# Kernel optimization log

Measured on AMD Instinct MI355X. Metric: run time of the kernel, lower is better.

## Reference

```python
import jax, jax.numpy as jnp
import numpy as np

B, N, D = 8, 2048, 512
S = 4096  # max_swaps


def setup_inputs() -> dict:
    key = jax.random.key(0)
    ks = jax.random.split(key, 5)
    h = jax.random.normal(ks[0], (B, N, D), dtype=jnp.float32)
    indices = jax.random.randint(ks[1], (B, S, 4), 0, N, dtype=jnp.int64)
    # MLP params (Linear stores weight as (out,in) in torch; we keep (in,out) and matmul)
    W1 = jax.random.normal(ks[2], (4 * D, D), dtype=jnp.float32) * (1.0 / np.sqrt(4 * D))
    b1 = jnp.zeros((D,), dtype=jnp.float32)
    W2 = jax.random.normal(ks[3], (D, D // 2), dtype=jnp.float32) * (1.0 / np.sqrt(D))
    b2 = jnp.zeros((D // 2,), dtype=jnp.float32)
    W3 = jax.random.normal(ks[4], (D // 2, 1), dtype=jnp.float32) * (1.0 / np.sqrt(D // 2))
    b3 = jnp.zeros((1,), dtype=jnp.float32)
    return {"h": h, "indices": indices, "W1": W1, "b1": b1, "W2": W2, "b2": b2, "W3": W3, "b3": b3}


def reference(h, indices, W1, b1, W2, b2, W3, b3):
    # h: (B, N, D); indices: (B, S, 4) node ids per swap
    swap_emb = jnp.take_along_axis(h[:, None, :, :], indices[..., None].astype(jnp.int32),
                                   axis=2)  # broadcast-gather -> (B, S, 4, D)
    # equivalently: h[batch_idx, indices]; implemented as per-batch gather
    swap_emb = jax.vmap(lambda hb, ib: hb[ib])(h, indices)  # (B, S, 4, D)
    swap_feats = swap_emb.reshape(h.shape[0], indices.shape[1], -1)  # (B, S, 4D)
    x = jax.nn.gelu(swap_feats @ W1 + b1, approximate=False)
    x = jax.nn.gelu(x @ W2 + b2, approximate=False)
    scores = (x @ W3 + b3)[..., 0]  # (B, S)
    rates = jax.nn.softplus(scores)
    return rates
```

## Files before the change

kernel.cpp:

```cpp
#include <hip/hip_runtime.h>
#include <math.h>

#define BATCH 8
#define NNODES 2048
#define DDIM 512
#define SWAPS 4096
#define M_TOTAL (BATCH * SWAPS)
#define KD DDIM
#define K2 DDIM
#define N2 (DDIM / 2)

typedef __attribute__((ext_vector_type(8))) __bf16 bf16x8;
typedef __attribute__((ext_vector_type(4))) float f32x4;
typedef __attribute__((ext_vector_type(8))) unsigned short us8;
typedef unsigned short ushort_t;

__device__ __forceinline__ float gelu_exact(float x) {
    return 0.5f * x * (1.0f + erff(x * 0.70710678118654752440f));
}
__device__ __forceinline__ float softplus_f(float x) {
    return fmaxf(x, 0.0f) + log1pf(expf(-fabsf(x)));
}
__device__ __forceinline__ unsigned short f2bf(float f) {
    unsigned int u = __builtin_bit_cast(unsigned int, f);
    u += 0x7FFFu + ((u >> 16) & 1u);
    return (unsigned short)(u >> 16);
}
__device__ __forceinline__ float bf2f(unsigned short s) {
    return __builtin_bit_cast(float, (unsigned int)s << 16);
}
__device__ __forceinline__ void glds16(const void* g, void* l) {
    __builtin_amdgcn_global_load_lds(
        (const __attribute__((address_space(1))) void*)g,
        (__attribute__((address_space(3))) void*)l, 16, 0, 0);
}

__global__ __launch_bounds__(256) void convert_kernel(
    const float* __restrict__ h, const float* __restrict__ W1,
    const float* __restrict__ W2, ushort_t* __restrict__ h_bf,
    ushort_t* __restrict__ W1pt, ushort_t* __restrict__ W2t)
{
    const int bid = blockIdx.x;
    if (bid < 8192) {
        size_t i = ((size_t)bid * 256 + threadIdx.x) * 4;
        float4 v = *(const float4*)(h + i);
        ushort4 o = { f2bf(v.x), f2bf(v.y), f2bf(v.z), f2bf(v.w) };
        *(ushort4*)(h_bf + i) = o;
    } else if (bid < 8192 + 1024) {
        size_t e = ((size_t)(bid - 8192) * 256 + threadIdx.x) * 4;
        const int k = (int)(e >> 9), n = (int)(e & 511);
        const int sg = k >> 9, d = k & 511;
        const int j = sg * 512 + n;
        float4 v = *(const float4*)(W1 + e);
        W1pt[(size_t)(j + 0) * KD + d] = f2bf(v.x);
        W1pt[(size_t)(j + 1) * KD + d] = f2bf(v.y);
        W1pt[(size_t)(j + 2) * KD + d] = f2bf(v.z);
        W1pt[(size_t)(j + 3) * KD + d] = f2bf(v.w);
    } else {
        size_t e = ((size_t)(bid - 9216) * 256 + threadIdx.x) * 4;
        const int k = (int)(e >> 8), n = (int)(e & 255);
        float4 v = *(const float4*)(W2 + e);
        W2t[(size_t)(n + 0) * K2 + k] = f2bf(v.x);
        W2t[(size_t)(n + 1) * K2 + k] = f2bf(v.y);
        W2t[(size_t)(n + 2) * K2 + k] = f2bf(v.z);
        W2t[(size_t)(n + 3) * K2 + k] = f2bf(v.w);
    }
}

__global__ __launch_bounds__(256) void gemm1_dense(
    const ushort_t* __restrict__ h_bf, const ushort_t* __restrict__ W1pt,
    ushort_t* __restrict__ P2)
{
    __shared__ __align__(16) char smem[32768];

    const int tid = threadIdx.x;
    const int w = tid >> 6, lane = tid & 63;
    const int quad = lane >> 4, l16 = lane & 15;
    const int wr = w >> 1, wc = w & 1;

    const int bid = blockIdx.x;
    const int xcd = bid & 7;
    const int r = bid >> 3;
    const int m0 = xcd * NNODES + (r & 15) * 128;
    const int n0 = (r >> 4) * 128;

    const int row0 = tid >> 2, sub = tid & 3;
    const int cg = (sub - (row0 >> 1)) & 3;
    const ushort_t* bA0 = h_bf + (size_t)(m0 + row0) * KD + cg * 8;
    const ushort_t* bA1 = h_bf + (size_t)(m0 + row0 + 64) * KD + cg * 8;
    const ushort_t* bB0 = W1pt + (size_t)(n0 + row0) * KD + cg * 8;
    const ushort_t* bB1 = W1pt + (size_t)(n0 + row0 + 64) * KD + cg * 8;

    int pa[4], pb[4];
    #pragma unroll
    for (int i = 0; i < 4; ++i) {
        const int rA = wr * 64 + i * 16 + l16;
        const int rB = wc * 64 + i * 16 + l16;
        pa[i] = rA * 64 + (((quad + (rA >> 1)) & 3) * 16);
        pb[i] = 8192 + rB * 64 + (((quad + (rB >> 1)) & 3) * 16);
    }

    f32x4 acc[4][4] = {};

    auto stage = [&](int kt, int half) {
        const int oo = kt * 32;
        char* base = smem + half * 16384;
        glds16(bA0 + oo, base + w * 1024);
        glds16(bA1 + oo, base + 4096 + w * 1024);
        glds16(bB0 + oo, base + 8192 + w * 1024);
        glds16(bB1 + oo, base + 12288 + w * 1024);
    };
    auto compute = [&](int half) {
        const char* base = smem + half * 16384;
        bf16x8 af[4], bfr[4];
        #pragma unroll
        for (int i = 0; i < 4; ++i) {
            af[i]  = *(const bf16x8*)(base + pa[i]);
            bfr[i] = *(const bf16x8*)(base + pb[i]);
        }
        #pragma unroll
        for (int i = 0; i < 4; ++i)
            #pragma unroll
            for (int jj = 0; jj < 4; ++jj)
                acc[i][jj] = __builtin_amdgcn_mfma_f32_16x16x32_bf16(
                    af[i], bfr[jj], acc[i][jj], 0, 0, 0);
    };

    for (int kt = 0; kt < 16; kt += 2) {
        stage(kt, 0);
        stage(kt + 1, 1);
        __syncthreads();
        compute(0);
        compute(1);
        __syncthreads();
    }

    #pragma unroll
    for (int jj = 0; jj < 4; ++jj) {
        const int j = n0 + wc * 64 + jj * 16 + l16;
        const int sg = j >> 9, nh = j & 511;
        const size_t base = ((size_t)(xcd * 2 + (nh >> 8)) * NNODES) * 1024
                          + (size_t)(sg << 8) + (nh & 255);
        #pragma unroll
        for (int i = 0; i < 4; ++i) {
            f32x4 v = acc[i][jj];
            #pragma unroll
            for (int rr = 0; rr < 4; ++rr) {
                const int node = (m0 + wr * 64 + i * 16 + quad * 4 + rr) & (NNODES - 1);
                P2[base + (size_t)node * 1024] = f2bf(v[rr]);
            }
        }
    }
}

__global__ __launch_bounds__(512) void fused_tail(
    const ushort_t* __restrict__ P2, const int* __restrict__ idx,
    const float* __restrict__ b1, const ushort_t* __restrict__ W2t,
    const float* __restrict__ b2, const float* __restrict__ W3,
    const float* __restrict__ b3, float* __restrict__ out)
{
    __shared__ __align__(16) char smem[40960];

    const int tid = threadIdx.x;
    const int w = tid >> 6, lane = tid & 63;
    const int quad = lane >> 4, l16 = lane & 15;
    const int rf = w >> 1, hf = w & 1;

    const int bid = blockIdx.x;
    const int b = bid & 7;
    const int m0 = b * SWAPS + (bid >> 3) * 64;

    const int arow = tid >> 2;
    const int ap = tid & 3;
    const int acg = (ap - (arow >> 1)) & 3;
    int4 iv = {0, 0, 0, 0};
    if (tid < 256) iv = *(const int4*)(idx + (size_t)(m0 + arow) * 4);
    const int nodes[4] = { iv.x, iv.y, iv.z, iv.w };
    const ushort_t* P2b = P2 + (size_t)(b * 2) * NNODES * 1024;

    const int vt = tid & 255;
    const int brow0 = vt >> 2, bsub = vt & 3;
    const int bcg = (bsub - (brow0 >> 1)) & 3;
    const ushort_t* pB[4];
    #pragma unroll
    for (int g = 0; g < 4; ++g)
        pB[g] = W2t + (size_t)(g * 64 + brow0) * K2 + bcg * 8;

    const int rA = rf * 16 + l16;
    const int paOff = rA * 64 + (((quad + (rA >> 1)) & 3) * 16);
    int pb[8];
    #pragma unroll
    for (int jf = 0; jf < 8; ++jf) {
        const int rB = hf * 128 + jf * 16 + l16;
        pb[jf] = 4096 + rB * 64 + (((quad + (rB >> 1)) & 3) * 16);
    }

    f32x4 acc[8] = {};

    auto stage = [&](int kc, int half) {
        char* base = smem + half * 20480;
        if (tid < 256) {
            const int nc = kc >> 3;
            const int pos0 = (kc & 7) * 32 + acg * 8;
            const ushort_t* Pr = P2b + (size_t)nc * NNODES * 1024;
            us8 v0 = *(const us8*)(Pr + (size_t)nodes[0] * 1024 + 0 * 256 + pos0);
            us8 v1 = *(const us8*)(Pr + (size_t)nodes[1] * 1024 + 1 * 256 + pos0);
            us8 v2 = *(const us8*)(Pr + (size_t)nodes[2] * 1024 + 2 * 256 + pos0);
            us8 v3 = *(const us8*)(Pr + (size_t)nodes[3] * 1024 + 3 * 256 + pos0);
            const float* bp = b1 + nc * 256 + pos0;
            float4 ba = *(const float4*)bp;
            float4 bb = *(const float4*)(bp + 4);
            float s[8] = { ba.x, ba.y, ba.z, ba.w, bb.x, bb.y, bb.z, bb.w };
            #pragma unroll
            for (int e = 0; e < 8; ++e)
                s[e] += bf2f(v0[e]) + bf2f(v1[e]) + bf2f(v2[e]) + bf2f(v3[e]);
            us8 o;
            #pragma unroll
            for (int e = 0; e < 8; ++e) o[e] = f2bf(gelu_exact(s[e]));
            *(us8*)(base + arow * 64 + ap * 16) = o;
        } else {
            const int oo = kc * 32;
            char* bbase = base + 4096;
            #pragma unroll
            for (int g = 0; g < 4; ++g)
                glds16(pB[g] + oo, bbase + g * 4096 + (w - 4) * 1024);
        }
    };
    auto compute = [&](int half) {
        const char* base = smem + half * 20480;
        bf16x8 af = *(const bf16x8*)(base + paOff);
        #pragma unroll
        for (int jf = 0; jf < 8; ++jf) {
            bf16x8 bfr = *(const bf16x8*)(base + pb[jf]);
            acc[jf] = __builtin_amdgcn_mfma_f32_16x16x32_bf16(af, bfr, acc[jf], 0, 0, 0);
        }
    };

    stage(0, 0);
    __syncthreads();
    for (int kc = 0; kc < 16; ++kc) {
        if (kc < 15) stage(kc + 1, (kc + 1) & 1);
        compute(kc & 1);
        __syncthreads();
    }

    float part[4] = {0.0f, 0.0f, 0.0f, 0.0f};
    #pragma unroll
    for (int jf = 0; jf < 8; ++jf) {
        const int n = hf * 128 + jf * 16 + l16;
        const float w3 = W3[n];
        const float bb2 = b2[n];
        f32x4 v = acc[jf];
        #pragma unroll
        for (int rr = 0; rr < 4; ++rr)
            part[rr] = fmaf(gelu_exact(v[rr] + bb2), w3, part[rr]);
    }
    #pragma unroll
    for (int off = 1; off < 16; off <<= 1)
        #pragma unroll
        for (int rr = 0; rr < 4; ++rr)
            part[rr] += __shfl_xor(part[rr], off);

    float* red = (float*)smem;
    if (hf == 1 && l16 == 0) {
        #pragma unroll
        for (int rr = 0; rr < 4; ++rr)
            red[rf * 16 + quad * 4 + rr] = part[rr];
    }
    __syncthreads();
    if (hf == 0 && l16 == 0) {
        const float bias3 = b3[0];
        #pragma unroll
        for (int rr = 0; rr < 4; ++rr) {
            const int r2 = rf * 16 + quad * 4 + rr;
            out[m0 + r2] = softplus_f(part[rr] + red[r2] + bias3);
        }
    }
}

extern "C" void kernel_launch(void* const* d_in, const int* in_sizes, int n_in,
                              void* d_out, int out_size, void* d_ws, size_t ws_size,
                              hipStream_t stream) {
    const float* h   = (const float*)d_in[0];
    const int*   idx = (const int*)d_in[1];
    const float* W1  = (const float*)d_in[2];
    const float* b1  = (const float*)d_in[3];
    const float* W2  = (const float*)d_in[4];
    const float* b2  = (const float*)d_in[5];
    const float* W3  = (const float*)d_in[6];
    const float* b3  = (const float*)d_in[7];
    float* out = (float*)d_out;

    char* ws = (char*)d_ws;
    ushort_t* P2    = (ushort_t*)ws;
    ushort_t* h_bf  = (ushort_t*)(ws + (64u << 20));
    ushort_t* W1pt  = (ushort_t*)(ws + (80u << 20));
    ushort_t* W2t   = (ushort_t*)(ws + (96u << 20));

    convert_kernel<<<9344, 256, 0, stream>>>(h, W1, W2, h_bf, W1pt, W2t);
    gemm1_dense<<<2048, 256, 0, stream>>>(h_bf, W1pt, P2);
    fused_tail<<<512, 512, 0, stream>>>(P2, idx, b1, W2t, b2, W3, b3, out);
}
```

Baseline: 189.0 us.

## Fuse h bf16 conversion into GEMM1 staging and use tanh GELU approximation

```diff
diff --git a/kernel.cpp b/kernel.cpp
--- a/kernel.cpp
+++ b/kernel.cpp
@@ -15,8 +15,12 @@
 typedef __attribute__((ext_vector_type(8))) unsigned short us8;
 typedef unsigned short ushort_t;
 
-__device__ __forceinline__ float gelu_exact(float x) {
-    return 0.5f * x * (1.0f + erff(x * 0.70710678118654752440f));
+__device__ __forceinline__ float gelu_fast(float x) {
+    const float u = 0.7978845608028654f * x * fmaf(0.044715f * x, x, 1.0f);
+    const float e = __expf(-2.0f * fabsf(u));
+    float t = (1.0f - e) / (1.0f + e);
+    t = copysignf(t, u);
+    return 0.5f * x * (1.0f + t);
 }
 __device__ __forceinline__ float softplus_f(float x) {
     return fmaxf(x, 0.0f) + log1pf(expf(-fabsf(x)));
@@ -36,18 +40,12 @@
 }
 
 __global__ __launch_bounds__(256) void convert_kernel(
-    const float* __restrict__ h, const float* __restrict__ W1,
-    const float* __restrict__ W2, ushort_t* __restrict__ h_bf,
+    const float* __restrict__ W1, const float* __restrict__ W2,
     ushort_t* __restrict__ W1pt, ushort_t* __restrict__ W2t)
 {
     const int bid = blockIdx.x;
-    if (bid < 8192) {
-        size_t i = ((size_t)bid * 256 + threadIdx.x) * 4;
-        float4 v = *(const float4*)(h + i);
-        ushort4 o = { f2bf(v.x), f2bf(v.y), f2bf(v.z), f2bf(v.w) };
-        *(ushort4*)(h_bf + i) = o;
-    } else if (bid < 8192 + 1024) {
-        size_t e = ((size_t)(bid - 8192) * 256 + threadIdx.x) * 4;
+    if (bid < 1024) {
+        size_t e = ((size_t)bid * 256 + threadIdx.x) * 4;
         const int k = (int)(e >> 9), n = (int)(e & 511);
         const int sg = k >> 9, d = k & 511;
         const int j = sg * 512 + n;
@@ -57,7 +55,7 @@
         W1pt[(size_t)(j + 2) * KD + d] = f2bf(v.z);
         W1pt[(size_t)(j + 3) * KD + d] = f2bf(v.w);
     } else {
-        size_t e = ((size_t)(bid - 9216) * 256 + threadIdx.x) * 4;
+        size_t e = ((size_t)(bid - 1024) * 256 + threadIdx.x) * 4;
         const int k = (int)(e >> 8), n = (int)(e & 255);
         float4 v = *(const float4*)(W2 + e);
         W2t[(size_t)(n + 0) * K2 + k] = f2bf(v.x);
@@ -68,7 +66,7 @@
 }
 
 __global__ __launch_bounds__(256) void gemm1_dense(
-    const ushort_t* __restrict__ h_bf, const ushort_t* __restrict__ W1pt,
+    const float* __restrict__ h, const ushort_t* __restrict__ W1pt,
     ushort_t* __restrict__ P2)
 {
     __shared__ __align__(16) char smem[32768];
@@ -86,8 +84,8 @@
 
     const int row0 = tid >> 2, sub = tid & 3;
     const int cg = (sub - (row0 >> 1)) & 3;
-    const ushort_t* bA0 = h_bf + (size_t)(m0 + row0) * KD + cg * 8;
-    const ushort_t* bA1 = h_bf + (size_t)(m0 + row0 + 64) * KD + cg * 8;
+    const float* fA0 = h + (size_t)(m0 + row0) * KD + cg * 8;
+    const float* fA1 = h + (size_t)(m0 + row0 + 64) * KD + cg * 8;
     const ushort_t* bB0 = W1pt + (size_t)(n0 + row0) * KD + cg * 8;
     const ushort_t* bB1 = W1pt + (size_t)(n0 + row0 + 64) * KD + cg * 8;
 
@@ -102,13 +100,25 @@
 
     f32x4 acc[4][4] = {};
 
-    auto stage = [&](int kt, int half) {
+    auto stageB = [&](int kt, int half) {
         const int oo = kt * 32;
         char* base = smem + half * 16384;
-        glds16(bA0 + oo, base + w * 1024);
-        glds16(bA1 + oo, base + 4096 + w * 1024);
         glds16(bB0 + oo, base + 8192 + w * 1024);
         glds16(bB1 + oo, base + 12288 + w * 1024);
+    };
+    auto stageA = [&](int kt, int half) {
+        char* base = smem + half * 16384;
+        const float* p0 = fA0 + kt * 32;
+        const float* p1 = fA1 + kt * 32;
+        float4 a0 = *(const float4*)p0, a1 = *(const float4*)(p0 + 4);
+        float4 c0 = *(const float4*)p1, c1 = *(const float4*)(p1 + 4);
+        us8 oA, oB;
+        oA[0] = f2bf(a0.x); oA[1] = f2bf(a0.y); oA[2] = f2bf(a0.z); oA[3] = f2bf(a0.w);
+        oA[4] = f2bf(a1.x); oA[5] = f2bf(a1.y); oA[6] = f2bf(a1.z); oA[7] = f2bf(a1.w);
+        oB[0] = f2bf(c0.x); oB[1] = f2bf(c0.y); oB[2] = f2bf(c0.z); oB[3] = f2bf(c0.w);
+        oB[4] = f2bf(c1.x); oB[5] = f2bf(c1.y); oB[6] = f2bf(c1.z); oB[7] = f2bf(c1.w);
+        *(us8*)(base + row0 * 64 + sub * 16) = oA;
+        *(us8*)(base + 4096 + row0 * 64 + sub * 16) = oB;
     };
     auto compute = [&](int half) {
         const char* base = smem + half * 16384;
@@ -127,8 +137,10 @@
     };
 
     for (int kt = 0; kt < 16; kt += 2) {
-        stage(kt, 0);
-        stage(kt + 1, 1);
+        stageB(kt, 0);
+        stageB(kt + 1, 1);
+        stageA(kt, 0);
+        stageA(kt + 1, 1);
         __syncthreads();
         compute(0);
         compute(1);
@@ -216,7 +228,7 @@
                 s[e] += bf2f(v0[e]) + bf2f(v1[e]) + bf2f(v2[e]) + bf2f(v3[e]);
             us8 o;
             #pragma unroll
-            for (int e = 0; e < 8; ++e) o[e] = f2bf(gelu_exact(s[e]));
+            for (int e = 0; e < 8; ++e) o[e] = f2bf(gelu_fast(s[e]));
             *(us8*)(base + arow * 64 + ap * 16) = o;
         } else {
             const int oo = kc * 32;
@@ -253,7 +265,7 @@
         f32x4 v = acc[jf];
         #pragma unroll
         for (int rr = 0; rr < 4; ++rr)
-            part[rr] = fmaf(gelu_exact(v[rr] + bb2), w3, part[rr]);
+            part[rr] = fmaf(gelu_fast(v[rr] + bb2), w3, part[rr]);
     }
     #pragma unroll
     for (int off = 1; off < 16; off <<= 1)
@@ -293,11 +305,10 @@
 
     char* ws = (char*)d_ws;
     ushort_t* P2    = (ushort_t*)ws;
-    ushort_t* h_bf  = (ushort_t*)(ws + (64u << 20));
-    ushort_t* W1pt  = (ushort_t*)(ws + (80u << 20));
-    ushort_t* W2t   = (ushort_t*)(ws + (96u << 20));
-
-    convert_kernel<<<9344, 256, 0, stream>>>(h, W1, W2, h_bf, W1pt, W2t);
-    gemm1_dense<<<2048, 256, 0, stream>>>(h_bf, W1pt, P2);
+    ushort_t* W1pt  = (ushort_t*)(ws + (64u << 20));
+    ushort_t* W2t   = (ushort_t*)(ws + (66u << 20));
+
+    convert_kernel<<<1152, 256, 0, stream>>>(W1, W2, W1pt, W2t);
+    gemm1_dense<<<2048, 256, 0, stream>>>(h, W1pt, P2);
     fused_tail<<<512, 512, 0, stream>>>(P2, idx, b1, W2t, b2, W3, b3, out);
 }
```

Result: no change. 187.9 us (-0.6%).
